# Kernel optimization log

Hardware: AMD Instinct MI355X
Metric: run time of the kernel (lower is better)

Reference implementation:

```python
import jax, jax.numpy as jnp
import numpy as np

B, T, D_IN, D_H1, D_H2, K = 8, 1024, 256, 1024, 1024, 9
EPS = 1e-12

def setup_inputs() -> dict:
    key = jax.random.key(0)
    ks = jax.random.split(key, 11)
    return {
        "x": jax.random.normal(ks[0], (B, T, D_IN), jnp.float32),
        "d_w": jax.random.normal(ks[1], (B, D_H1, 1, K), jnp.float32),
        "d_g": jax.random.uniform(ks[2], (B, D_H1), jnp.float32),
        "d_b": jax.random.normal(ks[3], (B, D_H1), jnp.float32) * 0.02,
        "p_w": jax.random.normal(ks[4], (B, D_H1, D_H2, 1), jnp.float32),
        "p_g": jax.random.uniform(ks[5], (B, D_H1), jnp.float32),
        "p_b": jax.random.normal(ks[6], (B, D_H2), jnp.float32) * 0.02,
        "w1_w": jax.random.normal(ks[7], (D_H1, D_IN), jnp.float32) / np.sqrt(D_IN),
        "w1_b": jnp.zeros((D_H1,), jnp.float32),
        "w2_w": jax.random.normal(ks[8], (D_IN, D_H2), jnp.float32) / np.sqrt(D_H2),
        "w2_b": jnp.zeros((D_IN,), jnp.float32),
    }

def _mish(v):
    return v * jnp.tanh(jax.nn.softplus(v))

def _wnorm(w, g):
    # F.normalize over channel dim 1, scaled by per-(batch,channel) gain g
    n = jnp.maximum(jnp.linalg.norm(w, axis=1, keepdims=True), EPS)
    return (w / n) * g[:, :, None, None]

def reference(x, d_w, d_g, d_b, p_w, p_g, p_b, w1_w, w1_b, w2_w, w2_b):
    residual = x
    # w_1: conv1x1 projection d_in -> d_hid1, channels-first [B, C, T]
    h = jnp.einsum('bti,ci->bct', x, w1_w) + w1_b[None, :, None]
    h = _mish(h)  # dropout is identity in eval
    k = d_w.shape[-1]
    p = (k - 1) // 2
    t = h.shape[-1]
    hp = jnp.pad(h, ((0, 0), (0, 0), (p, p)))
    # unfold: overlapping windows [B, C, T, K] (small fixed K loop)
    x_unf = jnp.stack([hp[:, :, i:i + t] for i in range(k)], axis=-1)
    dw = _wnorm(d_w, d_g)[:, :, 0, :]  # [B, C, K]
    y = jnp.einsum('bctk,bck->bct', x_unf, dw) + d_b[:, :, None]
    pw = _wnorm(p_w, p_g)[..., 0]      # [B, C, O]
    y = jnp.einsum('bct,bco->bot', y, pw) + p_b[:, :, None]
    # w_2: conv1x1 projection d_hid2 -> d_in, back to [B, T, d_in]
    out = jnp.einsum('bot,io->bti', y, w2_w) + w2_b
    return out + residual
```

## Files before the change

kernel.cpp:

```cpp
#include <hip/hip_runtime.h>
#include <hip/hip_bf16.h>

#define B_  8
#define T_  1024
#define DI_ 256
#define C_  1024
#define O_  1024
#define KW  9
#define BT_ 8192
#define EPSF 1e-12f

typedef unsigned short u16;
typedef u16   ushort8 __attribute__((ext_vector_type(8)));
typedef u16   ushort4v __attribute__((ext_vector_type(4)));
typedef __bf16 bf16x8 __attribute__((ext_vector_type(8)));
typedef float  f32x4  __attribute__((ext_vector_type(4)));

#define GLOAD_LDS16(g, l) __builtin_amdgcn_global_load_lds( \
    (const __attribute__((address_space(1))) void*)(g),      \
    (__attribute__((address_space(3))) void*)(l), 16, 0, 0)

__device__ __forceinline__ float bf2f(u16 u) {
    union { unsigned int i; float f; } z; z.i = ((unsigned int)u) << 16; return z.f;
}
__device__ __forceinline__ u16 f2bf(float f) {
    union { float f; unsigned int i; } z; z.f = f;
    unsigned int i = z.i;
    i += 0x7FFFu + ((i >> 16) & 1u);
    return (u16)(i >> 16);
}
__device__ __forceinline__ float mishf(float v) {
    float u = __expf(v);
    float w = 1.f + u;
    return v * (1.f - 2.f / (w * w + 1.f));
}

#define PB_XB 2048
#define PB_W1 2304
#define PB_W2 2560
#define PB_DN 2568
#define PB_PT 4616

__global__ __launch_bounds__(256)
void prep_k(const float* __restrict__ x,   u16* __restrict__ xb,
            const float* __restrict__ w1w, u16* __restrict__ w1b16,
            const float* __restrict__ w2w, u16* __restrict__ w2b16,
            const float* __restrict__ d_w, const float* __restrict__ d_g,
            float* __restrict__ dwf,
            const float* __restrict__ p_w, const float* __restrict__ p_g,
            float* __restrict__ part, u16* __restrict__ pwT)
{
    const int bid = blockIdx.x;
    const int tid = threadIdx.x;

    if (bid < PB_W2) {
        const float* in;
        u16* out;
        int i;
        if (bid < PB_XB)      { in = x;   out = xb;    i = bid * 256 + tid; }
        else if (bid < PB_W1) { in = w1w; out = w1b16; i = (bid - PB_XB) * 256 + tid; }
        else                  { in = w2w; out = w2b16; i = (bid - PB_W1) * 256 + tid; }
        float4 v = ((const float4*)in)[i];
        ushort4v o;
        o.x = f2bf(v.x); o.y = f2bf(v.y); o.z = f2bf(v.z); o.w = f2bf(v.w);
        ((ushort4v*)out)[i] = o;
    } else if (bid < PB_DN) {
        __shared__ float red[KW][256];
        __shared__ float nrm[KW];
        const int b = bid - PB_W2;
        float s[KW];
#pragma unroll
        for (int k = 0; k < KW; k++) s[k] = 0.f;
        for (int c = tid; c < C_; c += 256) {
#pragma unroll
            for (int k = 0; k < KW; k++) {
                float v = d_w[((size_t)b * C_ + c) * KW + k];
                s[k] += v * v;
            }
        }
#pragma unroll
        for (int k = 0; k < KW; k++) red[k][tid] = s[k];
        __syncthreads();
        if (tid < KW) {
            float t = 0.f;
            for (int i = 0; i < 256; i++) t += red[tid][i];
            nrm[tid] = fmaxf(sqrtf(t), EPSF);
        }
        __syncthreads();
        for (int c = tid; c < C_; c += 256) {
            float g = d_g[(size_t)b * C_ + c];
#pragma unroll
            for (int k = 0; k < KW; k++)
                dwf[((size_t)b * C_ + c) * KW + k] =
                    d_w[((size_t)b * C_ + c) * KW + k] / nrm[k] * g;
        }
    } else {
        __shared__ float ts[64][65];
        __shared__ float sq[4][64];
        const int idx = bid - PB_DN;
        const int b   = idx >> 8;
        const int rem = idx & 255;
        const int c0  = (rem >> 4) * 64, o0 = (rem & 15) * 64;
        const int col = tid & 63;
        const int rg  = tid >> 6;
        float ssq = 0.f;
        for (int r = rg; r < 64; r += 4) {
            float v = p_w[((size_t)b * C_ + c0 + r) * O_ + o0 + col];
            ssq += v * v;
            ts[r][col] = v * p_g[(size_t)b * C_ + c0 + r];
        }
        sq[rg][col] = ssq;
        __syncthreads();
        if (tid < 64)
            part[((size_t)b * 16 + (rem >> 4)) * O_ + o0 + tid] =
                sq[0][tid] + sq[1][tid] + sq[2][tid] + sq[3][tid];
        for (int r = rg; r < 64; r += 4)
            pwT[((size_t)b * O_ + o0 + r) * C_ + c0 + col] = f2bf(ts[col][r]);
    }
}

__global__ __launch_bounds__(256)
void dwconv_k(const u16* __restrict__ h, const float* __restrict__ dwf,
              const float* __restrict__ d_b, u16* __restrict__ y1gT)
{
    __shared__ u16 hs[64][74];
    const int b  = blockIdx.z;
    const int c0 = blockIdx.y * 64, t0 = blockIdx.x * 64;
    const int tid = threadIdx.x;
    for (int idx = tid; idx < 64 * 72; idx += 256) {
        int cc = idx / 72, tt = idx % 72;
        int t = t0 + tt - 4;
        u16 v = 0;
        if (t >= 0 && t < T_) v = h[(size_t)(c0 + cc) * BT_ + b * T_ + t];
        hs[cc][tt] = v;
    }
    __syncthreads();
    const int cc = tid & 63;
    const int c  = c0 + cc;
    float w[KW];
#pragma unroll
    for (int k = 0; k < KW; k++) w[k] = dwf[((size_t)b * C_ + c) * KW + k];
    const float bb = d_b[(size_t)b * C_ + c];
    for (int tt = tid >> 6; tt < 64; tt += 4) {
        float s = bb;
#pragma unroll
        for (int k = 0; k < KW; k++) s += bf2f(hs[cc][tt + k]) * w[k];
        y1gT[((size_t)b * T_ + t0 + tt) * C_ + c] = f2bf(s);
    }
}

template<int EPI, int TNF>
__global__ __launch_bounds__(256)
void gemm_nk(const u16* __restrict__ A, const u16* __restrict__ Bt,
             void* __restrict__ Dv, const float* __restrict__ bias,
             const float* __restrict__ extra,
             int M, int N, int Kd)
{
    __shared__ u16 As[2][128 * 64];
    __shared__ u16 Bs[2][TNF * 32 * 64];

    const int gx = gridDim.x;
    const unsigned nwg = (unsigned)gx * gridDim.y;
    unsigned lin = blockIdx.y * gx + blockIdx.x;
    lin = (lin & 7u) * (nwg >> 3) + (lin >> 3);
    const int m0 = (int)(lin / gx) * 128;
    const int n0 = (int)(lin % gx) * (TNF * 32);

    const int b = (EPI == 1) ? (m0 >> 10) : 0;
    if (EPI == 1) {
        Bt   += (size_t)b * O_ * C_;
        bias += (size_t)b * O_;
        extra+= (size_t)b * 16 * O_;
    }
    u16*   Db = (EPI == 2) ? nullptr : (u16*)Dv;
    float* Df = (EPI == 2) ? (float*)Dv : nullptr;
    const float* X = (EPI == 2) ? extra : nullptr;

    const int tid  = threadIdx.x;
    const int lane = tid & 63, wave = tid >> 6;
    const int wm = (wave & 1) * 64, wn = (wave >> 1) * (TNF * 16);
    const int lr = lane & 15;

    const int sbase = wave * 8;
    const int srowL = lane >> 3;
    const int scolE = ((lane & 7) ^ srowL) * 8;

    f32x4 acc[4][TNF];
#pragma unroll
    for (int i = 0; i < 4; i++)
#pragma unroll
        for (int j = 0; j < TNF; j++) acc[i][j] = (f32x4){0.f, 0.f, 0.f, 0.f};

    auto STAGE = [&](int buf, int k0) {
#pragma unroll
        for (int i = 0; i < 4; i++)
            GLOAD_LDS16(&A[(size_t)(m0 + i * 32 + sbase + srowL) * Kd + k0 + scolE],
                        &As[buf][(i * 32 + sbase) * 64]);
#pragma unroll
        for (int i = 0; i < TNF; i++)
            GLOAD_LDS16(&Bt[(size_t)(n0 + i * 32 + sbase + srowL) * Kd + k0 + scolE],
                        &Bs[buf][(i * 32 + sbase) * 64]);
    };

    const int NT = Kd >> 6;
    STAGE(0, 0);
    for (int kt = 0; kt < NT; kt++) {
        __syncthreads();
        if (kt + 1 < NT) STAGE((kt + 1) & 1, (kt + 1) << 6);
        const u16* as = As[kt & 1];
        const u16* bs = Bs[kt & 1];
        bf16x8 av[2][4], bv[2][TNF];
#pragma unroll
        for (int kk = 0; kk < 2; kk++) {
            const int slot = (lane >> 4) + kk * 4;
            const int sw = (slot ^ (lr & 7)) << 3;
#pragma unroll
            for (int i = 0; i < 4; i++)
                av[kk][i] = *(const bf16x8*)&as[(wm + i * 16 + lr) * 64 + sw];
#pragma unroll
            for (int j = 0; j < TNF; j++)
                bv[kk][j] = *(const bf16x8*)&bs[(wn + j * 16 + lr) * 64 + sw];
        }
#pragma unroll
        for (int kk = 0; kk < 2; kk++)
#pragma unroll
            for (int i = 0; i < 4; i++)
#pragma unroll
                for (int j = 0; j < TNF; j++)
                    acc[i][j] = __builtin_amdgcn_mfma_f32_16x16x32_bf16(
                        av[kk][i], bv[kk][j], acc[i][j], 0, 0, 0);
    }

    const int r0 = (lane >> 4) * 4;
#pragma unroll
    for (int i = 0; i < 4; i++) {
#pragma unroll
        for (int j = 0; j < TNF; j++) {
            const int col = n0 + wn + j * 16 + lr;
            float iv = 0.f;
            if (EPI == 1) {
                float s = 0.f;
#pragma unroll
                for (int ch = 0; ch < 16; ch++)
                    s += extra[(size_t)ch * O_ + col];
                iv = 1.f / fmaxf(sqrtf(s), EPSF);
            }
#pragma unroll
            for (int r = 0; r < 4; r++) {
                const int row = m0 + wm + i * 16 + r0 + r;
                float v = acc[i][j][r];
                if (EPI == 0) {
                    v += bias[row];
                    v = mishf(v);
                    Db[(size_t)row * N + col] = f2bf(v);
                } else if (EPI == 1) {
                    v = v * iv + bias[col];
                    Db[(size_t)row * N + col] = f2bf(v);
                } else {
                    v += bias[col] + X[(size_t)row * N + col];
                    Df[(size_t)row * N + col] = v;
                }
            }
        }
    }
}

extern "C" void kernel_launch(void* const* d_in, const int* in_sizes, int n_in,
                              void* d_out, int out_size, void* d_ws, size_t ws_size,
                              hipStream_t stream)
{
    const float* x   = (const float*)d_in[0];
    const float* d_w = (const float*)d_in[1];
    const float* d_g = (const float*)d_in[2];
    const float* d_b = (const float*)d_in[3];
    const float* p_w = (const float*)d_in[4];
    const float* p_g = (const float*)d_in[5];
    const float* p_b = (const float*)d_in[6];
    const float* w1w = (const float*)d_in[7];
    const float* w1b = (const float*)d_in[8];
    const float* w2w = (const float*)d_in[9];
    const float* w2b = (const float*)d_in[10];
    float* out = (float*)d_out;

    char* ws = (char*)d_ws;
    const size_t SZ = (size_t)16777216;
    u16*   h    = (u16*)(ws);
    u16*   y1gT = (u16*)(ws + SZ);
    u16*   pwT  = (u16*)(ws + 2 * SZ);
    u16*   y2T  = (u16*)(ws + 3 * SZ);
    u16*   xb   = (u16*)(ws + 4 * SZ);
    u16*   w1b16= (u16*)(ws + 4 * SZ + 4194304);
    u16*   w2b16= (u16*)(ws + 4 * SZ + 4718592);
    float* dwf  = (float*)(ws + 4 * SZ + 5242880);
    float* part = (float*)(ws + 4 * SZ + 5242880 + 294912);

    prep_k<<<dim3(PB_PT), 256, 0, stream>>>(
        x, xb, w1w, w1b16, w2w, w2b16, d_w, d_g, dwf, p_w, p_g, part, pwT);

    gemm_nk<0, 4><<<dim3(BT_ / 128, C_ / 128), 256, 0, stream>>>(
        w1b16, xb, h, w1b, nullptr, C_, BT_, DI_);

    dwconv_k<<<dim3(T_ / 64, C_ / 64, B_), 256, 0, stream>>>(h, dwf, d_b, y1gT);

    gemm_nk<1, 4><<<dim3(O_ / 128, BT_ / 128), 256, 0, stream>>>(
        y1gT, pwT, y2T, p_b, part, BT_, O_, C_);

    gemm_nk<2, 2><<<dim3(DI_ / 64, BT_ / 128), 256, 0, stream>>>(
        y2T, w2b16, out, w2b, x, BT_, DI_, O_);
}
```

Measured before the change: 102.5 us.

## Widen GEMM tiles to 128x256 with 32-deep K steps for first two GEMMs

The first two GEMMs now use a 128x256 output tile per block, with each wave computing 64x128 (4x8 MFMA accumulators), and a K step of 32 instead of 64 with a matching 4-way LDS swizzle. This raises arithmetic intensity per staged byte and cuts global and LDS traffic per FLOP. The cost is higher register pressure (128 accumulator floats per lane, launch_bounds set to 1 block), fewer blocks per GEMM, and twice as many K iterations, each with its own barrier. The third GEMM keeps the old tiling as a separate specialized kernel.

New measurement: 119.0 us. 1.16x slower.

```diff
diff --git a/kernel.cpp b/kernel.cpp
--- a/kernel.cpp
+++ b/kernel.cpp
@@ -149,93 +149,83 @@
     }
 }
 
-template<int EPI, int TNF>
-__global__ __launch_bounds__(256)
-void gemm_nk(const u16* __restrict__ A, const u16* __restrict__ Bt,
-             void* __restrict__ Dv, const float* __restrict__ bias,
-             const float* __restrict__ extra,
-             int M, int N, int Kd)
-{
-    __shared__ u16 As[2][128 * 64];
-    __shared__ u16 Bs[2][TNF * 32 * 64];
+template<int EPI>
+__device__ __forceinline__ void gemmw_body(
+    const u16* __restrict__ A, const u16* __restrict__ Bt,
+    u16* __restrict__ Db, const float* __restrict__ bias,
+    const float* __restrict__ extra, int M, int N, int Kd)
+{
+    __shared__ u16 As[2][128 * 32];
+    __shared__ u16 Bs[2][256 * 32];
 
     const int gx = gridDim.x;
     const unsigned nwg = (unsigned)gx * gridDim.y;
     unsigned lin = blockIdx.y * gx + blockIdx.x;
     lin = (lin & 7u) * (nwg >> 3) + (lin >> 3);
     const int m0 = (int)(lin / gx) * 128;
-    const int n0 = (int)(lin % gx) * (TNF * 32);
+    const int n0 = (int)(lin % gx) * 256;
 
     const int b = (EPI == 1) ? (m0 >> 10) : 0;
     if (EPI == 1) {
-        Bt   += (size_t)b * O_ * C_;
-        bias += (size_t)b * O_;
-        extra+= (size_t)b * 16 * O_;
-    }
-    u16*   Db = (EPI == 2) ? nullptr : (u16*)Dv;
-    float* Df = (EPI == 2) ? (float*)Dv : nullptr;
-    const float* X = (EPI == 2) ? extra : nullptr;
+        Bt    += (size_t)b * O_ * C_;
+        bias  += (size_t)b * O_;
+        extra += (size_t)b * 16 * O_;
+    }
 
     const int tid  = threadIdx.x;
     const int lane = tid & 63, wave = tid >> 6;
-    const int wm = (wave & 1) * 64, wn = (wave >> 1) * (TNF * 16);
+    const int wm = (wave >> 1) * 64, wn = (wave & 1) * 128;
     const int lr = lane & 15;
 
-    const int sbase = wave * 8;
-    const int srowL = lane >> 3;
-    const int scolE = ((lane & 7) ^ srowL) * 8;
-
-    f32x4 acc[4][TNF];
+    const int srow  = lane >> 2;
+    const int scolE = ((lane & 3) ^ (srow & 3)) * 8;
+
+    f32x4 acc[4][8];
 #pragma unroll
     for (int i = 0; i < 4; i++)
 #pragma unroll
-        for (int j = 0; j < TNF; j++) acc[i][j] = (f32x4){0.f, 0.f, 0.f, 0.f};
+        for (int j = 0; j < 8; j++) acc[i][j] = (f32x4){0.f, 0.f, 0.f, 0.f};
 
     auto STAGE = [&](int buf, int k0) {
 #pragma unroll
+        for (int i = 0; i < 2; i++)
+            GLOAD_LDS16(&A[(size_t)(m0 + i * 64 + wave * 16 + srow) * Kd + k0 + scolE],
+                        &As[buf][(i * 64 + wave * 16) * 32]);
+#pragma unroll
         for (int i = 0; i < 4; i++)
-            GLOAD_LDS16(&A[(size_t)(m0 + i * 32 + sbase + srowL) * Kd + k0 + scolE],
-                        &As[buf][(i * 32 + sbase) * 64]);
-#pragma unroll
-        for (int i = 0; i < TNF; i++)
-            GLOAD_LDS16(&Bt[(size_t)(n0 + i * 32 + sbase + srowL) * Kd + k0 + scolE],
-                        &Bs[buf][(i * 32 + sbase) * 64]);
+            GLOAD_LDS16(&Bt[(size_t)(n0 + i * 64 + wave * 16 + srow) * Kd + k0 + scolE],
+                        &Bs[buf][(i * 64 + wave * 16) * 32]);
     };
 
-    const int NT = Kd >> 6;
+    const int NT = Kd >> 5;
     STAGE(0, 0);
     for (int kt = 0; kt < NT; kt++) {
         __syncthreads();
-        if (kt + 1 < NT) STAGE((kt + 1) & 1, (kt + 1) << 6);
+        if (kt + 1 < NT) STAGE((kt + 1) & 1, (kt + 1) << 5);
         const u16* as = As[kt & 1];
         const u16* bs = Bs[kt & 1];
-        bf16x8 av[2][4], bv[2][TNF];
-#pragma unroll
-        for (int kk = 0; kk < 2; kk++) {
-            const int slot = (lane >> 4) + kk * 4;
-            const int sw = (slot ^ (lr & 7)) << 3;
-#pragma unroll
-            for (int i = 0; i < 4; i++)
-                av[kk][i] = *(const bf16x8*)&as[(wm + i * 16 + lr) * 64 + sw];
-#pragma unroll
-            for (int j = 0; j < TNF; j++)
-                bv[kk][j] = *(const bf16x8*)&bs[(wn + j * 16 + lr) * 64 + sw];
-        }
-#pragma unroll
-        for (int kk = 0; kk < 2; kk++)
-#pragma unroll
-            for (int i = 0; i < 4; i++)
-#pragma unroll
-                for (int j = 0; j < TNF; j++)
-                    acc[i][j] = __builtin_amdgcn_mfma_f32_16x16x32_bf16(
-                        av[kk][i], bv[kk][j], acc[i][j], 0, 0, 0);
+        const int slot = lane >> 4;
+        const int sw = (slot ^ (lr & 3)) << 3;
+        bf16x8 av[4], bv[8];
+#pragma unroll
+        for (int i = 0; i < 4; i++)
+            av[i] = *(const bf16x8*)&as[(wm + i * 16 + lr) * 32 + sw];
+#pragma unroll
+        for (int j = 0; j < 8; j++)
+            bv[j] = *(const bf16x8*)&bs[(wn + j * 16 + lr) * 32 + sw];
+#pragma unroll
+        for (int i = 0; i < 4; i++)
+#pragma unroll
+            for (int j = 0; j < 8; j++)
+                acc[i][j] = __builtin_amdgcn_mfma_f32_16x16x32_bf16(
+                    av[i], bv[j], acc[i][j], 0, 0, 0);
     }
 
     const int r0 = (lane >> 4) * 4;
 #pragma unroll
     for (int i = 0; i < 4; i++) {
 #pragma unroll
-        for (int j = 0; j < TNF; j++) {
+        for (int j = 0; j < 8; j++) {
             const int col = n0 + wn + j * 16 + lr;
             float iv = 0.f;
             if (EPI == 1) {
@@ -252,14 +242,112 @@
                 if (EPI == 0) {
                     v += bias[row];
                     v = mishf(v);
-                    Db[(size_t)row * N + col] = f2bf(v);
-                } else if (EPI == 1) {
+                } else {
                     v = v * iv + bias[col];
-                    Db[(size_t)row * N + col] = f2bf(v);
-                } else {
-                    v += bias[col] + X[(size_t)row * N + col];
-                    Df[(size_t)row * N + col] = v;
                 }
+                Db[(size_t)row * N + col] = f2bf(v);
+            }
+        }
+    }
+}
+
+__global__ __launch_bounds__(256, 1)
+void gemm1_k(const u16* __restrict__ A, const u16* __restrict__ Bt,
+             u16* __restrict__ D, const float* __restrict__ bias,
+             int M, int N, int Kd)
+{
+    gemmw_body<0>(A, Bt, D, bias, nullptr, M, N, Kd);
+}
+
+__global__ __launch_bounds__(256, 1)
+void gemm2_k(const u16* __restrict__ A, const u16* __restrict__ Bt,
+             u16* __restrict__ D, const float* __restrict__ bias,
+             const float* __restrict__ extra, int M, int N, int Kd)
+{
+    gemmw_body<1>(A, Bt, D, bias, extra, M, N, Kd);
+}
+
+__global__ __launch_bounds__(256)
+void gemm3_k(const u16* __restrict__ A, const u16* __restrict__ Bt,
+             float* __restrict__ Df, const float* __restrict__ bias,
+             const float* __restrict__ X, int M, int N, int Kd)
+{
+    __shared__ u16 As[2][128 * 64];
+    __shared__ u16 Bs[2][64 * 64];
+
+    const int gx = gridDim.x;
+    const unsigned nwg = (unsigned)gx * gridDim.y;
+    unsigned lin = blockIdx.y * gx + blockIdx.x;
+    lin = (lin & 7u) * (nwg >> 3) + (lin >> 3);
+    const int m0 = (int)(lin / gx) * 128;
+    const int n0 = (int)(lin % gx) * 64;
+
+    const int tid  = threadIdx.x;
+    const int lane = tid & 63, wave = tid >> 6;
+    const int wm = (wave & 1) * 64, wn = (wave >> 1) * 32;
+    const int lr = lane & 15;
+
+    const int sbase = wave * 8;
+    const int srowL = lane >> 3;
+    const int scolE = ((lane & 7) ^ srowL) * 8;
+
+    f32x4 acc[4][2];
+#pragma unroll
+    for (int i = 0; i < 4; i++)
+#pragma unroll
+        for (int j = 0; j < 2; j++) acc[i][j] = (f32x4){0.f, 0.f, 0.f, 0.f};
+
+    auto STAGE = [&](int buf, int k0) {
+#pragma unroll
+        for (int i = 0; i < 4; i++)
+            GLOAD_LDS16(&A[(size_t)(m0 + i * 32 + sbase + srowL) * Kd + k0 + scolE],
+                        &As[buf][(i * 32 + sbase) * 64]);
+#pragma unroll
+        for (int i = 0; i < 2; i++)
+            GLOAD_LDS16(&Bt[(size_t)(n0 + i * 32 + sbase + srowL) * Kd + k0 + scolE],
+                        &Bs[buf][(i * 32 + sbase) * 64]);
+    };
+
+    const int NT = Kd >> 6;
+    STAGE(0, 0);
+    for (int kt = 0; kt < NT; kt++) {
+        __syncthreads();
+        if (kt + 1 < NT) STAGE((kt + 1) & 1, (kt + 1) << 6);
+        const u16* as = As[kt & 1];
+        const u16* bs = Bs[kt & 1];
+        bf16x8 av[2][4], bv[2][2];
+#pragma unroll
+        for (int kk = 0; kk < 2; kk++) {
+            const int slot = (lane >> 4) + kk * 4;
+            const int sw = (slot ^ (lr & 7)) << 3;
+#pragma unroll
+            for (int i = 0; i < 4; i++)
+                av[kk][i] = *(const bf16x8*)&as[(wm + i * 16 + lr) * 64 + sw];
+#pragma unroll
+            for (int j = 0; j < 2; j++)
+                bv[kk][j] = *(const bf16x8*)&bs[(wn + j * 16 + lr) * 64 + sw];
+        }
+#pragma unroll
+        for (int kk = 0; kk < 2; kk++)
+#pragma unroll
+            for (int i = 0; i < 4; i++)
+#pragma unroll
+                for (int j = 0; j < 2; j++)
+                    acc[i][j] = __builtin_amdgcn_mfma_f32_16x16x32_bf16(
+                        av[kk][i], bv[kk][j], acc[i][j], 0, 0, 0);
+    }
+
+    const int r0 = (lane >> 4) * 4;
+#pragma unroll
+    for (int i = 0; i < 4; i++) {
+#pragma unroll
+        for (int j = 0; j < 2; j++) {
+            const int col = n0 + wn + j * 16 + lr;
+#pragma unroll
+            for (int r = 0; r < 4; r++) {
+                const int row = m0 + wm + i * 16 + r0 + r;
+                Df[(size_t)row * N + col] =
+                    acc[i][j][r] + bias[col] + X[(size_t)row * N + col];
             }
         }
     }
@@ -297,14 +385,14 @@
     prep_k<<<dim3(PB_PT), 256, 0, stream>>>(
         x, xb, w1w, w1b16, w2w, w2b16, d_w, d_g, dwf, p_w, p_g, part, pwT);
 
-    gemm_nk<0, 4><<<dim3(BT_ / 128, C_ / 128), 256, 0, stream>>>(
-        w1b16, xb, h, w1b, nullptr, C_, BT_, DI_);
+    gemm1_k<<<dim3(BT_ / 256, C_ / 128), 256, 0, stream>>>(
+        w1b16, xb, h, w1b, C_, BT_, DI_);
 
     dwconv_k<<<dim3(T_ / 64, C_ / 64, B_), 256, 0, stream>>>(h, dwf, d_b, y1gT);
 
-    gemm_nk<1, 4><<<dim3(O_ / 128, BT_ / 128), 256, 0, stream>>>(
+    gemm2_k<<<dim3(O_ / 256, BT_ / 128), 256, 0, stream>>>(
         y1gT, pwT, y2T, p_b, part, BT_, O_, C_);
 
-    gemm_nk<2, 2><<<dim3(DI_ / 64, BT_ / 128), 256, 0, stream>>>(
+    gemm3_k<<<dim3(DI_ / 64, BT_ / 128), 256, 0, stream>>>(
         y2T, w2b16, out, w2b, x, BT_, DI_, O_);
 }
```

## Triple-buffer GEMM LDS with K=32 tiles and explicit vmcnt waits

Applied to the files above, without the earlier changes.

Reworks the shared GEMM main loop from a double-buffered 64-wide K tile to a triple-buffered 32-wide K tile. Loads are prefetched two stages ahead, and __syncthreads is replaced with targeted s_waitcnt vmcnt plus s_barrier, so global-to-LDS transfers overlap compute more deeply. LDS use per block shrinks, and launch bounds now request 3 blocks per CU to raise occupancy. The cost is more barriers per unit of K and a hand-counted vmcnt that must stay in step with the number of loads issued.

Result: slower. 106.3 us (+3.6%).

```diff
diff --git a/kernel.cpp b/kernel.cpp
--- a/kernel.cpp
+++ b/kernel.cpp
@@ -150,14 +150,13 @@
 }
 
 template<int EPI, int TNF>
-__global__ __launch_bounds__(256)
-void gemm_nk(const u16* __restrict__ A, const u16* __restrict__ Bt,
-             void* __restrict__ Dv, const float* __restrict__ bias,
-             const float* __restrict__ extra,
-             int M, int N, int Kd)
-{
-    __shared__ u16 As[2][128 * 64];
-    __shared__ u16 Bs[2][TNF * 32 * 64];
+__device__ __forceinline__ void gemm_body(
+    const u16* __restrict__ A, const u16* __restrict__ Bt,
+    void* __restrict__ Dv, const float* __restrict__ bias,
+    const float* __restrict__ extra, int M, int N, int Kd)
+{
+    __shared__ u16 As[3 * 4096];
+    __shared__ u16 Bs[3 * 1024 * TNF];
 
     const int gx = gridDim.x;
     const unsigned nwg = (unsigned)gx * gridDim.y;
@@ -168,9 +167,9 @@
 
     const int b = (EPI == 1) ? (m0 >> 10) : 0;
     if (EPI == 1) {
-        Bt   += (size_t)b * O_ * C_;
-        bias += (size_t)b * O_;
-        extra+= (size_t)b * 16 * O_;
+        Bt    += (size_t)b * O_ * C_;
+        bias  += (size_t)b * O_;
+        extra += (size_t)b * 16 * O_;
     }
     u16*   Db = (EPI == 2) ? nullptr : (u16*)Dv;
     float* Df = (EPI == 2) ? (float*)Dv : nullptr;
@@ -180,10 +179,10 @@
     const int lane = tid & 63, wave = tid >> 6;
     const int wm = (wave & 1) * 64, wn = (wave >> 1) * (TNF * 16);
     const int lr = lane & 15;
-
-    const int sbase = wave * 8;
-    const int srowL = lane >> 3;
-    const int scolE = ((lane & 7) ^ srowL) * 8;
+    const int q  = lane >> 4;
+    const int srow  = lane >> 2;
+    const int scolE = ((lane & 3) ^ (srow & 3)) * 8;
+    const int sw    = (q ^ (lr & 3)) << 3;
 
     f32x4 acc[4][TNF];
 #pragma unroll
@@ -191,44 +190,49 @@
 #pragma unroll
         for (int j = 0; j < TNF; j++) acc[i][j] = (f32x4){0.f, 0.f, 0.f, 0.f};
 
-    auto STAGE = [&](int buf, int k0) {
+    auto STAGE = [&](int buf, int kt) {
+        const int k0 = kt << 5;
+#pragma unroll
+        for (int i = 0; i < 2; i++)
+            GLOAD_LDS16(&A[(size_t)(m0 + i * 64 + wave * 16 + srow) * Kd + k0 + scolE],
+                        &As[buf * 4096 + (i * 64 + wave * 16) * 32]);
+#pragma unroll
+        for (int i = 0; i < TNF / 2; i++)
+            GLOAD_LDS16(&Bt[(size_t)(n0 + i * 64 + wave * 16 + srow) * Kd + k0 + scolE],
+                        &Bs[buf * (1024 * TNF) + (i * 64 + wave * 16) * 32]);
+    };
+
+    const int NT = Kd >> 5;
+    STAGE(0, 0);
+    STAGE(1, 1);
+    int rb = 0, sb = 2;
+    for (int kt = 0; kt < NT; kt++) {
+        if (kt == NT - 1) {
+            asm volatile("s_waitcnt vmcnt(0)" ::: "memory");
+        } else if constexpr (TNF == 4) {
+            asm volatile("s_waitcnt vmcnt(4)" ::: "memory");
+        } else {
+            asm volatile("s_waitcnt vmcnt(3)" ::: "memory");
+        }
+        __builtin_amdgcn_s_barrier();
+        if (kt + 2 < NT) STAGE(sb, kt + 2);
+        const u16* as = &As[rb * 4096];
+        const u16* bs = &Bs[rb * (1024 * TNF)];
+        bf16x8 av[4], bv[TNF];
 #pragma unroll
         for (int i = 0; i < 4; i++)
-            GLOAD_LDS16(&A[(size_t)(m0 + i * 32 + sbase + srowL) * Kd + k0 + scolE],
-                        &As[buf][(i * 32 + sbase) * 64]);
-#pragma unroll
-        for (int i = 0; i < TNF; i++)
-            GLOAD_LDS16(&Bt[(size_t)(n0 + i * 32 + sbase + srowL) * Kd + k0 + scolE],
-                        &Bs[buf][(i * 32 + sbase) * 64]);
-    };
-
-    const int NT = Kd >> 6;
-    STAGE(0, 0);
-    for (int kt = 0; kt < NT; kt++) {
-        __syncthreads();
-        if (kt + 1 < NT) STAGE((kt + 1) & 1, (kt + 1) << 6);
-        const u16* as = As[kt & 1];
-        const u16* bs = Bs[kt & 1];
-        bf16x8 av[2][4], bv[2][TNF];
-#pragma unroll
-        for (int kk = 0; kk < 2; kk++) {
-            const int slot = (lane >> 4) + kk * 4;
-            const int sw = (slot ^ (lr & 7)) << 3;
-#pragma unroll
-            for (int i = 0; i < 4; i++)
-                av[kk][i] = *(const bf16x8*)&as[(wm + i * 16 + lr) * 64 + sw];
+            av[i] = *(const bf16x8*)&as[(wm + i * 16 + lr) * 32 + sw];
+#pragma unroll
+        for (int j = 0; j < TNF; j++)
+            bv[j] = *(const bf16x8*)&bs[(wn + j * 16 + lr) * 32 + sw];
+#pragma unroll
+        for (int i = 0; i < 4; i++)
 #pragma unroll
             for (int j = 0; j < TNF; j++)
-                bv[kk][j] = *(const bf16x8*)&bs[(wn + j * 16 + lr) * 64 + sw];
-        }
-#pragma unroll
-        for (int kk = 0; kk < 2; kk++)
-#pragma unroll
-            for (int i = 0; i < 4; i++)
-#pragma unroll
-                for (int j = 0; j < TNF; j++)
-                    acc[i][j] = __builtin_amdgcn_mfma_f32_16x16x32_bf16(
-                        av[kk][i], bv[kk][j], acc[i][j], 0, 0, 0);
+                acc[i][j] = __builtin_amdgcn_mfma_f32_16x16x32_bf16(
+                    av[i], bv[j], acc[i][j], 0, 0, 0);
+        rb = (rb == 2) ? 0 : rb + 1;
+        sb = (sb == 2) ? 0 : sb + 1;
     }
 
     const int r0 = (lane >> 4) * 4;
@@ -265,6 +269,30 @@
     }
 }
 
+__global__ __launch_bounds__(256, 3)
+void gemm1_k(const u16* __restrict__ A, const u16* __restrict__ Bt,
+             u16* __restrict__ D, const float* __restrict__ bias,
+             int M, int N, int Kd)
+{
+    gemm_body<0, 4>(A, Bt, D, bias, nullptr, M, N, Kd);
+}
+
+__global__ __launch_bounds__(256, 3)
+void gemm2_k(const u16* __restrict__ A, const u16* __restrict__ Bt,
+             u16* __restrict__ D, const float* __restrict__ bias,
+             const float* __restrict__ extra, int M, int N, int Kd)
+{
+    gemm_body<1, 4>(A, Bt, D, bias, extra, M, N, Kd);
+}
+
+__global__ __launch_bounds__(256, 3)
+void gemm3_k(const u16* __restrict__ A, const u16* __restrict__ Bt,
+             float* __restrict__ D, const float* __restrict__ bias,
+             const float* __restrict__ X, int M, int N, int Kd)
+{
+    gemm_body<2, 2>(A, Bt, (void*)D, bias, X, M, N, Kd);
+}
+
 extern "C" void kernel_launch(void* const* d_in, const int* in_sizes, int n_in,
                               void* d_out, int out_size, void* d_ws, size_t ws_size,
                               hipStream_t stream)
@@ -297,14 +325,14 @@
     prep_k<<<dim3(PB_PT), 256, 0, stream>>>(
         x, xb, w1w, w1b16, w2w, w2b16, d_w, d_g, dwf, p_w, p_g, part, pwT);
 
-    gemm_nk<0, 4><<<dim3(BT_ / 128, C_ / 128), 256, 0, stream>>>(
-        w1b16, xb, h, w1b, nullptr, C_, BT_, DI_);
+    gemm1_k<<<dim3(BT_ / 128, C_ / 128), 256, 0, stream>>>(
+        w1b16, xb, h, w1b, C_, BT_, DI_);
 
     dwconv_k<<<dim3(T_ / 64, C_ / 64, B_), 256, 0, stream>>>(h, dwf, d_b, y1gT);
 
-    gemm_nk<1, 4><<<dim3(O_ / 128, BT_ / 128), 256, 0, stream>>>(
+    gemm2_k<<<dim3(O_ / 128, BT_ / 128), 256, 0, stream>>>(
         y1gT, pwT, y2T, p_b, part, BT_, O_, C_);
 
-    gemm_nk<2, 2><<<dim3(DI_ / 64, BT_ / 128), 256, 0, stream>>>(
+    gemm3_k<<<dim3(DI_ / 64, BT_ / 128), 256, 0, stream>>>(
         y2T, w2b16, out, w2b, x, BT_, DI_, O_);
 }
```
